# Kernel optimization log

Hardware: AMD Instinct MI355X
Metric: run time of the kernel (lower is better)

## Reference

```python
import jax, jax.numpy as jnp
import numpy as np

N_NODES = 100000
N_EDGES = 1600000
IN_F = 256
OUT_F = 128


def setup_inputs() -> dict:
    key = jax.random.key(0)
    k1, k2, k3, k4, k5 = jax.random.split(key, 5)
    x = jax.random.normal(k1, (N_NODES, IN_F), dtype=jnp.float32)
    edge_rows = jax.random.randint(k2, (N_EDGES,), 0, N_NODES, dtype=jnp.int32)
    edge_cols = jax.random.randint(k3, (N_EDGES,), 0, N_NODES, dtype=jnp.int32)
    edge_vals = jax.random.uniform(k4, (N_EDGES,), dtype=jnp.float32)
    # glorot init for weight, zeros for bias (matches reset_parameters)
    limit = float(np.sqrt(6.0 / (IN_F + OUT_F)))
    weight = jax.random.uniform(k5, (IN_F, OUT_F), dtype=jnp.float32,
                                minval=-limit, maxval=limit)
    bias = jnp.zeros((OUT_F,), dtype=jnp.float32)
    return {"x": x, "edge_rows": edge_rows, "edge_cols": edge_cols,
            "edge_vals": edge_vals, "weight": weight, "bias": bias}


def reference(x, edge_rows, edge_cols, edge_vals, weight, bias):
    # dense projection: [N, in] @ [in, out] -> [N, out]
    h = x @ weight
    # spmm(adj, h): out[r] = sum_{edges e with row r} vals[e] * h[col[e]]
    msgs = edge_vals[:, None] * h[edge_cols]          # [E, out]
    agg = jax.ops.segment_sum(msgs, edge_rows, num_segments=N_NODES)
    return agg + bias
```

## Files before the change

kernel.cpp:

```cpp
#include <hip/hip_runtime.h>


typedef __attribute__((ext_vector_type(8))) short short8;
typedef __attribute__((ext_vector_type(4))) float floatx4;
typedef __attribute__((ext_vector_type(2))) int intv2;

#define WT_K 264
#define GM_NODES 128
#define BSHIFT 6
#define BROWS 64
#define CAP 1280
#define NBMAX 1600
#define EPB 6400
#define CSH 4
#define OVFCAP 65536

static __device__ __forceinline__ uint f2bf(float x) {
  uint u = __float_as_uint(x);
  return (u + 0x7fffu + ((u >> 16) & 1u)) >> 16;
}

__global__ __launch_bounds__(256) void conv_w(const float* __restrict__ w,
                                              ushort* __restrict__ wt,
                                              int* __restrict__ cursors,
                                              int n_ints) {
  const int f = blockIdx.x;
  const int k = threadIdx.x;
  wt[f * WT_K + k] = (ushort)f2bf(w[k * 128 + f]);
  for (int i = blockIdx.x * 256 + threadIdx.x; i < n_ints; i += 128 * 256)
    cursors[i] = 0;
}

__global__ __launch_bounds__(256) void gemm_mfma(const float* __restrict__ x,
                                                 const ushort* __restrict__ wt,
                                                 ushort* __restrict__ h,
                                                 int n_nodes) {
  __shared__ ushort lw[128 * WT_K];
  __shared__ ushort xa[GM_NODES * 40];
  const int t = threadIdx.x;
  const int lane = t & 63;
  const int wq = t >> 6;
  const int quad = lane >> 4;
  const int l15 = lane & 15;
  const int row0 = blockIdx.x * GM_NODES;

  {
    const uint4* src = (const uint4*)wt;
    uint4* dst = (uint4*)lw;
    for (int i = t; i < (128 * WT_K * 2) / 16; i += 256) dst[i] = src[i];
  }

  floatx4 acc[2][8];
#pragma unroll
  for (int nt = 0; nt < 2; ++nt)
#pragma unroll
    for (int mt = 0; mt < 8; ++mt) acc[nt][mt] = (floatx4){0.f, 0.f, 0.f, 0.f};

  float4 cur[4];
#pragma unroll
  for (int i = 0; i < 4; ++i) {
    const int idx = i * 256 + t;
    const int row = idx >> 3, kq = idx & 7;
    const int gr = row0 + row;
    cur[i] = (gr < n_nodes) ? *(const float4*)&x[(size_t)gr * 256 + kq * 4]
                            : make_float4(0.f, 0.f, 0.f, 0.f);
  }

  for (int kc = 0; kc < 8; ++kc) {
#pragma unroll
    for (int i = 0; i < 4; ++i) {
      const int idx = i * 256 + t;
      const int row = idx >> 3, kq = idx & 7;
      uint2 p;
      p.x = f2bf(cur[i].x) | (f2bf(cur[i].y) << 16);
      p.y = f2bf(cur[i].z) | (f2bf(cur[i].w) << 16);
      *(uint2*)&xa[row * 40 + kq * 4] = p;
    }
    __syncthreads();

    float4 nxt[4];
    if (kc < 7) {
#pragma unroll
      for (int i = 0; i < 4; ++i) {
        const int idx = i * 256 + t;
        const int row = idx >> 3, kq = idx & 7;
        const int gr = row0 + row;
        nxt[i] = (gr < n_nodes)
                     ? *(const float4*)&x[(size_t)gr * 256 + (kc + 1) * 32 + kq * 4]
                     : make_float4(0.f, 0.f, 0.f, 0.f);
      }
    }

    short8 bfr[2];
    bfr[0] = *(const short8*)&xa[(wq * 32 + l15) * 40 + quad * 8];
    bfr[1] = *(const short8*)&xa[(wq * 32 + 16 + l15) * 40 + quad * 8];
#pragma unroll
    for (int mt = 0; mt < 8; ++mt) {
      const short8 afr =
          *(const short8*)&lw[(mt * 16 + l15) * WT_K + kc * 32 + quad * 8];
      acc[0][mt] = __builtin_amdgcn_mfma_f32_16x16x32_bf16(afr, bfr[0],
                                                           acc[0][mt], 0, 0, 0);
      acc[1][mt] = __builtin_amdgcn_mfma_f32_16x16x32_bf16(afr, bfr[1],
                                                           acc[1][mt], 0, 0, 0);
    }
    __syncthreads();
#pragma unroll
    for (int i = 0; i < 4; ++i) cur[i] = nxt[i];
  }

#pragma unroll
  for (int nt = 0; nt < 2; ++nt) {
    const int node = row0 + wq * 32 + nt * 16 + l15;
    if (node < n_nodes) {
#pragma unroll
      for (int mt = 0; mt < 8; ++mt) {
        uint2 p;
        p.x = f2bf(acc[nt][mt][0]) | (f2bf(acc[nt][mt][1]) << 16);
        p.y = f2bf(acc[nt][mt][2]) | (f2bf(acc[nt][mt][3]) << 16);
        *(uint2*)&h[(size_t)node * 128 + mt * 16 + quad * 4] = p;
      }
    }
  }
}

__global__ __launch_bounds__(256) void fill_bin(
    const int* __restrict__ erows, const int* __restrict__ ecols,
    const float* __restrict__ evals, int* __restrict__ cursors,
    int2* __restrict__ bcv, int* __restrict__ ovf_cnt,
    int4* __restrict__ ovf, int n_edges, int nb) {
  __shared__ int2 rec[EPB];
  __shared__ short bkt[EPB];
  __shared__ int cnt[NBMAX], bas[NBMAX], cur[NBMAX];
  const int t = threadIdx.x;
  const int e0 = blockIdx.x * EPB;
  const int n = min(EPB, n_edges - e0);
  if (n <= 0) return;

  for (int b = t; b < nb; b += 256) { cnt[b] = 0; cur[b] = 0; }
  __syncthreads();

  {
    int i = t;
    for (; i + 768 < n; i += 1024) {
      int r0 = __builtin_nontemporal_load(&erows[e0 + i]);
      int r1 = __builtin_nontemporal_load(&erows[e0 + i + 256]);
      int r2 = __builtin_nontemporal_load(&erows[e0 + i + 512]);
      int r3 = __builtin_nontemporal_load(&erows[e0 + i + 768]);
      int c0 = __builtin_nontemporal_load(&ecols[e0 + i]);
      int c1 = __builtin_nontemporal_load(&ecols[e0 + i + 256]);
      int c2 = __builtin_nontemporal_load(&ecols[e0 + i + 512]);
      int c3 = __builtin_nontemporal_load(&ecols[e0 + i + 768]);
      float v0 = __builtin_nontemporal_load(&evals[e0 + i]);
      float v1 = __builtin_nontemporal_load(&evals[e0 + i + 256]);
      float v2 = __builtin_nontemporal_load(&evals[e0 + i + 512]);
      float v3 = __builtin_nontemporal_load(&evals[e0 + i + 768]);
      int2 p0; p0.x = c0 | ((r0 & (BROWS - 1)) << 17); p0.y = __float_as_int(v0);
      int2 p1; p1.x = c1 | ((r1 & (BROWS - 1)) << 17); p1.y = __float_as_int(v1);
      int2 p2; p2.x = c2 | ((r2 & (BROWS - 1)) << 17); p2.y = __float_as_int(v2);
      int2 p3; p3.x = c3 | ((r3 & (BROWS - 1)) << 17); p3.y = __float_as_int(v3);
      rec[i] = p0; rec[i + 256] = p1; rec[i + 512] = p2; rec[i + 768] = p3;
      const int b0 = r0 >> BSHIFT, b1 = r1 >> BSHIFT;
      const int b2 = r2 >> BSHIFT, b3 = r3 >> BSHIFT;
      bkt[i] = (short)b0; bkt[i + 256] = (short)b1;
      bkt[i + 512] = (short)b2; bkt[i + 768] = (short)b3;
      atomicAdd(&cnt[b0], 1); atomicAdd(&cnt[b1], 1);
      atomicAdd(&cnt[b2], 1); atomicAdd(&cnt[b3], 1);
    }
    for (; i < n; i += 256) {
      const int r = __builtin_nontemporal_load(&erows[e0 + i]);
      const int c = __builtin_nontemporal_load(&ecols[e0 + i]);
      const float v = __builtin_nontemporal_load(&evals[e0 + i]);
      int2 p; p.x = c | ((r & (BROWS - 1)) << 17); p.y = __float_as_int(v);
      rec[i] = p;
      const int b = r >> BSHIFT;
      bkt[i] = (short)b;
      atomicAdd(&cnt[b], 1);
    }
  }
  __syncthreads();

  for (int b = t; b < nb; b += 256) {
    const int c = cnt[b];
    if (c > 0) bas[b] = atomicAdd(&cursors[b << CSH], c);
  }
  __syncthreads();

  for (int i = t; i < n; i += 256) {
    const int b = (int)bkt[i];
    const int loc = atomicAdd(&cur[b], 1);
    const int pos = bas[b] + loc;
    const int2 p = rec[i];
    if (pos < CAP) {
      bcv[(size_t)b * CAP + pos] = p;
    } else {
      int op = atomicAdd(ovf_cnt, 1);
      if (op < OVFCAP) {
        int4 q;
        q.x = (b << BSHIFT) | ((p.x >> 17) & (BROWS - 1));
        q.y = p.x & 0x1FFFF;
        q.z = p.y; q.w = 0;
        ovf[op] = q;
      }
    }
  }
}

__global__ __launch_bounds__(256) void sort_gather(
    const ushort* __restrict__ h, const int* __restrict__ cursors,
    const int2* __restrict__ bcv, const float* __restrict__ bias,
    float* __restrict__ out, int n_nodes, int nb) {
  __shared__ int2 buf[CAP];
  __shared__ int cnt[BROWS], start[BROWS], cur[BROWS];
  const int b = blockIdx.x;
  const int t = threadIdx.x;
  const int nrec = min(cursors[b << CSH], CAP);
  if (t < BROWS) cnt[t] = 0;
  __syncthreads();

  const int2* src = &bcv[(size_t)b * CAP];
  for (int i = t; i < nrec; i += 256) atomicAdd(&cnt[((uint)src[i].x) >> 17], 1);
  __syncthreads();

  if (t < BROWS) {
    int c = cnt[t];
    int s = c;
#pragma unroll
    for (int off = 1; off < 64; off <<= 1) {
      int u = __shfl_up(s, off, 64);
      if (t >= off) s += u;
    }
    start[t] = s - c;
    cur[t] = s - c;
  }
  __syncthreads();

  for (int i = t; i < nrec; i += 256) {
    intv2 rr = __builtin_nontemporal_load((const intv2*)&src[i]);
    int2 recv; recv.x = rr[0]; recv.y = rr[1];
    int pos = atomicAdd(&cur[((uint)recv.x) >> 17], 1);
    buf[pos] = recv;
  }
  __syncthreads();

  const int lane = t & 63;
  const int w = t >> 6;
  const float2 bv = ((const float2*)bias)[lane];
  for (int rr = w * 16; rr < w * 16 + 16; ++rr) {
    const int node = b * BROWS + rr;
    if (node >= n_nodes) break;
    float2 acca = bv;
    float2 accb = make_float2(0.f, 0.f);
    int p = start[rr];
    const int p1 = start[rr] + cnt[rr];
    for (; p + 8 <= p1; p += 8) {
      int2 e0 = buf[p + 0];
      int2 e1 = buf[p + 1];
      int2 e2 = buf[p + 2];
      int2 e3 = buf[p + 3];
      int2 e4 = buf[p + 4];
      int2 e5 = buf[p + 5];
      int2 e6 = buf[p + 6];
      int2 e7 = buf[p + 7];
      uint u0 = ((const uint*)(h + (size_t)(e0.x & 0x1FFFF) * 128))[lane];
      uint u1 = ((const uint*)(h + (size_t)(e1.x & 0x1FFFF) * 128))[lane];
      uint u2 = ((const uint*)(h + (size_t)(e2.x & 0x1FFFF) * 128))[lane];
      uint u3 = ((const uint*)(h + (size_t)(e3.x & 0x1FFFF) * 128))[lane];
      uint u4 = ((const uint*)(h + (size_t)(e4.x & 0x1FFFF) * 128))[lane];
      uint u5 = ((const uint*)(h + (size_t)(e5.x & 0x1FFFF) * 128))[lane];
      uint u6 = ((const uint*)(h + (size_t)(e6.x & 0x1FFFF) * 128))[lane];
      uint u7 = ((const uint*)(h + (size_t)(e7.x & 0x1FFFF) * 128))[lane];
      float v0 = __int_as_float(e0.y), v1 = __int_as_float(e1.y);
      float v2 = __int_as_float(e2.y), v3 = __int_as_float(e3.y);
      float v4 = __int_as_float(e4.y), v5 = __int_as_float(e5.y);
      float v6 = __int_as_float(e6.y), v7 = __int_as_float(e7.y);
      acca.x += v0 * __uint_as_float(u0 << 16);
      acca.y += v0 * __uint_as_float(u0 & 0xffff0000u);
      accb.x += v1 * __uint_as_float(u1 << 16);
      accb.y += v1 * __uint_as_float(u1 & 0xffff0000u);
      acca.x += v2 * __uint_as_float(u2 << 16);
      acca.y += v2 * __uint_as_float(u2 & 0xffff0000u);
      accb.x += v3 * __uint_as_float(u3 << 16);
      accb.y += v3 * __uint_as_float(u3 & 0xffff0000u);
      acca.x += v4 * __uint_as_float(u4 << 16);
      acca.y += v4 * __uint_as_float(u4 & 0xffff0000u);
      accb.x += v5 * __uint_as_float(u5 << 16);
      accb.y += v5 * __uint_as_float(u5 & 0xffff0000u);
      acca.x += v6 * __uint_as_float(u6 << 16);
      acca.y += v6 * __uint_as_float(u6 & 0xffff0000u);
      accb.x += v7 * __uint_as_float(u7 << 16);
      accb.y += v7 * __uint_as_float(u7 & 0xffff0000u);
    }
    for (; p < p1; ++p) {
      int2 ev = buf[p];
      float v = __int_as_float(ev.y);
      uint u = ((const uint*)(h + (size_t)(ev.x & 0x1FFFF) * 128))[lane];
      acca.x += v * __uint_as_float(u << 16);
      acca.y += v * __uint_as_float(u & 0xffff0000u);
    }
    float2 accf;
    accf.x = acca.x + accb.x;
    accf.y = acca.y + accb.y;
    ((float2*)(out + (size_t)node * 128))[lane] = accf;
  }
}

__global__ __launch_bounds__(256) void ovf_scatter(
    const ushort* __restrict__ h, const int* __restrict__ ovf_cnt,
    const int4* __restrict__ ovf, float* __restrict__ out) {
  const int n = min(*ovf_cnt, OVFCAP);
  const int lane = threadIdx.x & 63;
  const int wid = (blockIdx.x * 256 + threadIdx.x) >> 6;
  const int nw = gridDim.x * 4;
  for (int e = wid; e < n; e += nw) {
    int4 recq = ovf[e];
    float v = __int_as_float(recq.z);
    uint u = ((const uint*)(h + (size_t)recq.y * 128))[lane];
    float* op = out + (size_t)recq.x * 128 + lane * 2;
    atomicAdd(op, v * __uint_as_float(u << 16));
    atomicAdd(op + 1, v * __uint_as_float(u & 0xffff0000u));
  }
}

__global__ __launch_bounds__(256) void init_bias(float* __restrict__ out,
                                                 const float* __restrict__ bias,
                                                 int n4) {
  int i = blockIdx.x * 256 + threadIdx.x;
  if (i < n4) {
    float4 b = ((const float4*)bias)[i & 31];
    ((float4*)out)[i] = b;
  }
}

__global__ __launch_bounds__(256) void scatter_edges(
    const ushort* __restrict__ h, const int* __restrict__ erows,
    const int* __restrict__ ecols, const float* __restrict__ evals,
    float* __restrict__ out, int n_edges) {
  int e = blockIdx.x * 4 + (threadIdx.x >> 6);
  if (e >= n_edges) return;
  int lane = threadIdx.x & 63;
  int row = erows[e];
  int col = ecols[e];
  float v = evals[e];
  uint u = ((const uint*)(h + (size_t)col * 128))[lane];
  float* op = out + (size_t)row * 128 + lane * 2;
  atomicAdd(op, v * __uint_as_float(u << 16));
  atomicAdd(op + 1, v * __uint_as_float(u & 0xffff0000u));
}

extern "C" void kernel_launch(void* const* d_in, const int* in_sizes, int n_in,
                              void* d_out, int out_size, void* d_ws, size_t ws_size,
                              hipStream_t stream) {
  const float* x     = (const float*)d_in[0];
  const int*   erows = (const int*)d_in[1];
  const int*   ecols = (const int*)d_in[2];
  const float* evals = (const float*)d_in[3];
  const float* w     = (const float*)d_in[4];
  const float* bias  = (const float*)d_in[5];
  float* out = (float*)d_out;

  const int n_nodes = in_sizes[0] / 256;
  const int n_edges = in_sizes[1];
  const int nb_buckets = (n_nodes + BROWS - 1) >> BSHIFT;

  char* ws = (char*)d_ws;
  size_t off = 0;
  ushort* h  = (ushort*)(ws + off);  off += ((size_t)n_nodes * 128 * 2 + 255) & ~255ull;
  ushort* wt = (ushort*)(ws + off);  off += ((size_t)128 * WT_K * 2 + 255) & ~255ull;
  const size_t cur_ints = (((size_t)nb_buckets) << CSH) + 16;
  int* cursors = (int*)(ws + off);   off += (cur_ints * 4 + 255) & ~255ull;
  int2* bcv    = (int2*)(ws + off);  off += ((size_t)nb_buckets * CAP * 8 + 255) & ~255ull;
  int4* ovf    = (int4*)(ws + off);  off += (size_t)OVFCAP * 16;
  const bool bucket_ok = (off <= ws_size) && (nb_buckets <= NBMAX) &&
                         (n_nodes <= 102400);
  int* ovf_cnt = cursors + (((size_t)nb_buckets) << CSH);

  const int zero_ints = bucket_ok ? (int)cur_ints : 0;
  conv_w<<<128, 256, 0, stream>>>(w, wt, cursors, zero_ints);
  const int gemm_blocks = (n_nodes + GM_NODES - 1) / GM_NODES;
  gemm_mfma<<<gemm_blocks, 256, 0, stream>>>(x, wt, h, n_nodes);

  if (bucket_ok) {
    const int eblocks = (n_edges + EPB - 1) / EPB;
    fill_bin<<<eblocks, 256, 0, stream>>>(erows, ecols, evals, cursors, bcv,
                                          ovf_cnt, ovf, n_edges, nb_buckets);
    sort_gather<<<nb_buckets, 256, 0, stream>>>(h, cursors, bcv, bias, out,
                                                n_nodes, nb_buckets);
    ovf_scatter<<<32, 256, 0, stream>>>(h, ovf_cnt, ovf, out);
  } else {
    const int n4 = out_size / 4;
    init_bias<<<(n4 + 255) / 256, 256, 0, stream>>>(out, bias, n4);
    scatter_edges<<<(n_edges + 3) / 4, 256, 0, stream>>>(h, erows, ecols, evals,
                                                         out, n_edges);
  }
}
```

Before: 302.5 us.

## Load GEMM B-fragments directly from global; keep bin records in registers

The GEMM kernel no longer stages x through a shared-memory tile. Each lane loads the 8 floats it needs for its MFMA B fragment straight from global memory, converts them to bf16 in registers, and drops two barriers per k-chunk. The sort_gather kernel reads each bin's records into registers once (up to 5 per thread, matching CAP=1280) instead of reading global memory twice for counting and scattering. The risks are less-coalesced global loads in the GEMM (32-byte per-lane rows) and higher register pressure. The code also contains a stray unused variable with a non-ASCII name.

```diff
diff --git a/kernel.cpp b/kernel.cpp
--- a/kernel.cpp
+++ b/kernel.cpp
@@ -20,6 +20,8 @@
   return (u + 0x7fffu + ((u >> 16) & 1u)) >> 16;
 }
 
+union u4s8 { uint4 u; short8 s; };
+
 __global__ __launch_bounds__(256) void conv_w(const float* __restrict__ w,
                                               ushort* __restrict__ wt,
                                               int* __restrict__ cursors,
@@ -36,7 +38,6 @@
                                                  ushort* __restrict__ h,
                                                  int n_nodes) {
   __shared__ ushort lw[128 * WT_K];
-  __shared__ ushort xa[GM_NODES * 40];
   const int t = threadIdx.x;
   const int lane = t & 63;
   const int wq = t >> 6;
@@ -56,56 +57,52 @@
 #pragma unroll
     for (int mt = 0; mt < 8; ++mt) acc[nt][mt] = (floatx4){0.f, 0.f, 0.f, 0.f};
 
-  float4 cur[4];
-#pragma unroll
-  for (int i = 0; i < 4; ++i) {
-    const int idx = i * 256 + t;
-    const int row = idx >> 3, kq = idx & 7;
-    const int gr = row0 + row;
-    cur[i] = (gr < n_nodes) ? *(const float4*)&x[(size_t)gr * 256 + kq * 4]
-                            : make_float4(0.f, 0.f, 0.f, 0.f);
-  }
+  const int n0 = row0 + wq * 32 + l15;
+  const int n1 = n0 + 16;
+  const bool v0 = (n0 < n_nodes), v1 = (n1 < n_nodes);
+  const float* p0 = x + (size_t)(v0 ? n0 : 0) * 256 + quad * 8;
+  const float* p1 = x + (size_t)(v1 ? n1 : 0) * 256 + quad * 8;
+  const float4 z4 = make_float4(0.f, 0.f, 0.f, 0.f);
+
+  float4 cா[4];
+  float4 cur0a = v0 ? *(const float4*)(p0 + 0) : z4;
+  float4 cur0b = v0 ? *(const float4*)(p0 + 4) : z4;
+  float4 cur1a = v1 ? *(const float4*)(p1 + 0) : z4;
+  float4 cur1b = v1 ? *(const float4*)(p1 + 4) : z4;
+  (void)cா;
+
+  __syncthreads();
 
   for (int kc = 0; kc < 8; ++kc) {
-#pragma unroll
-    for (int i = 0; i < 4; ++i) {
-      const int idx = i * 256 + t;
-      const int row = idx >> 3, kq = idx & 7;
-      uint2 p;
-      p.x = f2bf(cur[i].x) | (f2bf(cur[i].y) << 16);
-      p.y = f2bf(cur[i].z) | (f2bf(cur[i].w) << 16);
-      *(uint2*)&xa[row * 40 + kq * 4] = p;
-    }
-    __syncthreads();
-
-    float4 nxt[4];
+    float4 nxt0a, nxt0b, nxt1a, nxt1b;
     if (kc < 7) {
-#pragma unroll
-      for (int i = 0; i < 4; ++i) {
-        const int idx = i * 256 + t;
-        const int row = idx >> 3, kq = idx & 7;
-        const int gr = row0 + row;
-        nxt[i] = (gr < n_nodes)
-                     ? *(const float4*)&x[(size_t)gr * 256 + (kc + 1) * 32 + kq * 4]
-                     : make_float4(0.f, 0.f, 0.f, 0.f);
-      }
-    }
-
-    short8 bfr[2];
-    bfr[0] = *(const short8*)&xa[(wq * 32 + l15) * 40 + quad * 8];
-    bfr[1] = *(const short8*)&xa[(wq * 32 + 16 + l15) * 40 + quad * 8];
+      const int o = (kc + 1) * 32;
+      nxt0a = v0 ? *(const float4*)(p0 + o + 0) : z4;
+      nxt0b = v0 ? *(const float4*)(p0 + o + 4) : z4;
+      nxt1a = v1 ? *(const float4*)(p1 + o + 0) : z4;
+      nxt1b = v1 ? *(const float4*)(p1 + o + 4) : z4;
+    }
+
+    u4s8 bf0, bf1;
+    bf0.u.x = f2bf(cur0a.x) | (f2bf(cur0a.y) << 16);
+    bf0.u.y = f2bf(cur0a.z) | (f2bf(cur0a.w) << 16);
+    bf0.u.z = f2bf(cur0b.x) | (f2bf(cur0b.y) << 16);
+    bf0.u.w = f2bf(cur0b.z) | (f2bf(cur0b.w) << 16);
+    bf1.u.x = f2bf(cur1a.x) | (f2bf(cur1a.y) << 16);
+    bf1.u.y = f2bf(cur1a.z) | (f2bf(cur1a.w) << 16);
+    bf1.u.z = f2bf(cur1b.x) | (f2bf(cur1b.y) << 16);
+    bf1.u.w = f2bf(cur1b.z) | (f2bf(cur1b.w) << 16);
+
 #pragma unroll
     for (int mt = 0; mt < 8; ++mt) {
       const short8 afr =
           *(const short8*)&lw[(mt * 16 + l15) * WT_K + kc * 32 + quad * 8];
-      acc[0][mt] = __builtin_amdgcn_mfma_f32_16x16x32_bf16(afr, bfr[0],
+      acc[0][mt] = __builtin_amdgcn_mfma_f32_16x16x32_bf16(afr, bf0.s,
                                                            acc[0][mt], 0, 0, 0);
-      acc[1][mt] = __builtin_amdgcn_mfma_f32_16x16x32_bf16(afr, bfr[1],
+      acc[1][mt] = __builtin_amdgcn_mfma_f32_16x16x32_bf16(afr, bf1.s,
                                                            acc[1][mt], 0, 0, 0);
     }
-    __syncthreads();
-#pragma unroll
-    for (int i = 0; i < 4; ++i) cur[i] = nxt[i];
+    cur0a = nxt0a; cur0b = nxt0b; cur1a = nxt1a; cur1b = nxt1b;
   }
 
 #pragma unroll
@@ -218,7 +215,22 @@
   __syncthreads();
 
   const int2* src = &bcv[(size_t)b * CAP];
-  for (int i = t; i < nrec; i += 256) atomicAdd(&cnt[((uint)src[i].x) >> 17], 1);
+  int2 r[5];
+#pragma unroll
+  for (int j = 0; j < 5; ++j) {
+    const int i = t + j * 256;
+    if (i < nrec) {
+      intv2 rv = __builtin_nontemporal_load((const intv2*)&src[i]);
+      r[j].x = rv[0]; r[j].y = rv[1];
+    } else {
+      r[j].x = 0; r[j].y = 0;
+    }
+  }
+#pragma unroll
+  for (int j = 0; j < 5; ++j) {
+    const int i = t + j * 256;
+    if (i < nrec) atomicAdd(&cnt[((uint)r[j].x) >> 17], 1);
+  }
   __syncthreads();
 
   if (t < BROWS) {
@@ -234,11 +246,13 @@
   }
   __syncthreads();
 
-  for (int i = t; i < nrec; i += 256) {
-    intv2 rr = __builtin_nontemporal_load((const intv2*)&src[i]);
-    int2 recv; recv.x = rr[0]; recv.y = rr[1];
-    int pos = atomicAdd(&cur[((uint)recv.x) >> 17], 1);
-    buf[pos] = recv;
+#pragma unroll
+  for (int j = 0; j < 5; ++j) {
+    const int i = t + j * 256;
+    if (i < nrec) {
+      int pos = atomicAdd(&cur[((uint)r[j].x) >> 17], 1);
+      buf[pos] = r[j];
+    }
   }
   __syncthreads();
 
```

Measured after the change: 299.4 us. No clear change (-1.0%).
